# Kernel tuning notes

Measured on AMD Instinct MI355X. Metric: run time of the kernel, lower is better.

Reference implementation:

```python
import jax, jax.numpy as jnp
import numpy as np
from jax import lax

B, S, D, H_HEADS, K, G, E, HID = 2, 1024, 1024, 16, 31, 4, 2, 2048
HD = D // H_HEADS

def _layer_norm(x, g, b, eps=1e-5):
    mu = jnp.mean(x, axis=-1, keepdims=True)
    var = jnp.mean(jnp.square(x - mu), axis=-1, keepdims=True)
    return (x - mu) * lax.rsqrt(var + eps) * g + b

def setup_inputs() -> dict:
    key = jax.random.key(0)
    ks = jax.random.split(key, 16)
    s = 0.02
    return {
        "x": jax.random.normal(ks[0], (B, S, D), jnp.float32),
        "group_ids": jax.random.randint(ks[1], (B, S), 0, G, jnp.int32),
        "cn_g": jnp.ones((D,), jnp.float32), "cn_b": jnp.zeros((D,), jnp.float32),
        "conv_w": jax.random.normal(ks[2], (D, D, K), jnp.float32) * s,
        "conv_b": jnp.zeros((D,), jnp.float32),
        "an_g": jnp.ones((D,), jnp.float32), "an_b": jnp.zeros((D,), jnp.float32),
        "in_w": jax.random.normal(ks[3], (3 * D, D), jnp.float32) * s,
        "in_b": jnp.zeros((3 * D,), jnp.float32),
        "out_w": jax.random.normal(ks[4], (D, D), jnp.float32) * s,
        "out_b": jnp.zeros((D,), jnp.float32),
        "e_w1": jax.random.normal(ks[5], (G, E, D, HID), jnp.float32) * s,
        "e_b1": jnp.zeros((G, E, HID), jnp.float32),
        "e_w2": jax.random.normal(ks[6], (G, E, HID, D), jnp.float32) * s,
        "e_b2": jnp.zeros((G, E, D), jnp.float32),
    }

def reference(x, group_ids, cn_g, cn_b, conv_w, conv_b, an_g, an_b,
              in_w, in_b, out_w, out_b, e_w1, e_b1, e_w2, e_b2):
    # ---- conv block (dropout off: deterministic/eval) ----
    residual = x
    h = _layer_norm(x, cn_g, cn_b)
    hc = jnp.transpose(h, (0, 2, 1))  # [B, D, S]
    hc = lax.conv_general_dilated(hc, conv_w, window_strides=(1,),
                                  padding=[(K // 2, K // 2)],
                                  dimension_numbers=("NCH", "OIH", "NCH"))
    hc = hc + conv_b[None, :, None]
    hc = jnp.transpose(hc, (0, 2, 1))
    x = jax.nn.gelu(hc, approximate=False) + residual
    # ---- self-attention block ----
    residual = x
    h = _layer_norm(x, an_g, an_b)
    qkv = h @ in_w.T + in_b  # [B, S, 3D]
    q, k, v = jnp.split(qkv, 3, axis=-1)
    q = q.reshape(B, S, H_HEADS, HD)
    k = k.reshape(B, S, H_HEADS, HD)
    v = v.reshape(B, S, H_HEADS, HD)
    scores = jnp.einsum("bqhd,bkhd->bhqk", q, k) / jnp.sqrt(jnp.float32(HD))
    attn = jax.nn.softmax(scores, axis=-1)
    ctx = jnp.einsum("bhqk,bkhd->bqhd", attn, v).reshape(B, S, D)
    x = ctx @ out_w.T + out_b + residual
    # ---- group-routed MoE (dense compute over groups, select by group id) ----
    residual = x
    xf = x.reshape(B * S, D)
    gid = group_ids.reshape(B * S)
    h1 = jax.nn.gelu(jnp.einsum("nd,gedh->ngeh", xf, e_w1) + e_b1, approximate=False)
    out_all = jnp.einsum("ngeh,gehd->nged", h1, e_w2) + e_b2  # [N, G, E, D]
    out_all = jnp.mean(out_all, axis=2)  # mean over experts in group -> [N, G, D]
    sel = jnp.take_along_axis(out_all, gid[:, None, None].astype(jnp.int32), axis=1)[:, 0]
    x = sel.reshape(B, S, D) + residual
    return x
```

## Files before the change

kernel.cpp:

```cpp
#include <hip/hip_runtime.h>
#include <hip/hip_bf16.h>
#include <math.h>

#define BB 2
#define SS 1024
#define DD 1024
#define HH 16
#define HDIM 64
#define KK 31
#define GG 4
#define EE 2
#define HIDN 2048
#define NTOK (BB*SS)
#define D3 (3*DD)

typedef unsigned short u16;
typedef __attribute__((ext_vector_type(8))) short s16x8;
typedef __attribute__((ext_vector_type(8))) unsigned short u16x8;
typedef __attribute__((ext_vector_type(4))) unsigned short u16x4;
typedef __attribute__((ext_vector_type(4))) float f32x4;
typedef __attribute__((ext_vector_type(2))) unsigned int u32x2;

__device__ __forceinline__ float gelu_f(float x) {
  return 0.5f * x * (1.0f + erff(x * 0.7071067811865475f));
}
__device__ __forceinline__ u16 f2bf(float f) {
  unsigned u = __builtin_bit_cast(unsigned, f);
  u = (u + 0x7fffu + ((u >> 16) & 1u)) >> 16;
  return (u16)u;
}
__device__ __forceinline__ float bf2f(u16 u) {
  return __builtin_bit_cast(float, ((unsigned)u) << 16);
}
__device__ __forceinline__ f32x4 MFMA16(s16x8 a, s16x8 b, f32x4 c) {
  return __builtin_amdgcn_mfma_f32_16x16x32_bf16(a, b, c, 0, 0, 0);
}
#define GLOAD16(gp, lp) __builtin_amdgcn_global_load_lds( \
    (const __attribute__((address_space(1))) void*)(gp),  \
    (__attribute__((address_space(3))) void*)(lp), 16, 0, 0)

__global__ void ln_kernel(const float* __restrict__ x, const float* __restrict__ g,
                          const float* __restrict__ b, u16* __restrict__ out) {
  const int row = blockIdx.x;
  const int tid = threadIdx.x;
  __shared__ float red[4];
  const float4 v = reinterpret_cast<const float4*>(x + (size_t)row * DD)[tid];
  float s = v.x + v.y + v.z + v.w;
  s += __shfl_down(s, 32); s += __shfl_down(s, 16); s += __shfl_down(s, 8);
  s += __shfl_down(s, 4);  s += __shfl_down(s, 2);  s += __shfl_down(s, 1);
  if ((tid & 63) == 0) red[tid >> 6] = s;
  __syncthreads();
  const float mean = (red[0] + red[1] + red[2] + red[3]) * (1.0f / DD);
  __syncthreads();
  const float4 d = make_float4(v.x - mean, v.y - mean, v.z - mean, v.w - mean);
  float sq = d.x*d.x + d.y*d.y + d.z*d.z + d.w*d.w;
  sq += __shfl_down(sq, 32); sq += __shfl_down(sq, 16); sq += __shfl_down(sq, 8);
  sq += __shfl_down(sq, 4);  sq += __shfl_down(sq, 2);  sq += __shfl_down(sq, 1);
  if ((tid & 63) == 0) red[tid >> 6] = sq;
  __syncthreads();
  const float var = (red[0] + red[1] + red[2] + red[3]) * (1.0f / DD);
  const float rstd = rsqrtf(var + 1e-5f);
  const float4 gv = reinterpret_cast<const float4*>(g)[tid];
  const float4 bv = reinterpret_cast<const float4*>(b)[tid];
  u16x4 o;
  o[0] = f2bf(d.x * rstd * gv.x + bv.x);
  o[1] = f2bf(d.y * rstd * gv.y + bv.y);
  o[2] = f2bf(d.z * rstd * gv.z + bv.z);
  o[3] = f2bf(d.w * rstd * gv.w + bv.w);
  *reinterpret_cast<u16x4*>(out + (size_t)row * DD + tid * 4) = o;
}

__global__ void prep_convw(const float* __restrict__ cw, u16* __restrict__ Wb) {
  const int o = blockIdx.x;
#pragma unroll
  for (int rep = 0; rep < 4; ++rep) {
    const int i = rep * 256 + threadIdx.x;
    const float* src = cw + ((size_t)o * DD + i) * KK;
    float wv[KK];
#pragma unroll
    for (int k = 0; k < KK; ++k) wv[k] = src[k];
#pragma unroll
    for (int k = 0; k < KK; ++k)
      Wb[((size_t)k * DD + o) * DD + i] = f2bf(wv[k]);
  }
}

__global__ void cvt_kernel(const float* __restrict__ in, u16* __restrict__ outp, int n4) {
  const int i = blockIdx.x * 256 + threadIdx.x;
  if (i < n4) {
    const float4 v = reinterpret_cast<const float4*>(in)[i];
    u16x4 o; o[0] = f2bf(v.x); o[1] = f2bf(v.y); o[2] = f2bf(v.z); o[3] = f2bf(v.w);
    reinterpret_cast<u16x4*>(outp)[i] = o;
  }
}

__global__ void tr_kernel(const float* __restrict__ src, u16* __restrict__ dst, int R, int C) {
  __shared__ float tile[32][33];
  const int c0 = blockIdx.x * 32, r0 = blockIdx.y * 32;
  const size_t base = (size_t)blockIdx.z * R * C;
  const int tx = threadIdx.x & 31, ty = threadIdx.x >> 5;
#pragma unroll
  for (int i = 0; i < 4; ++i)
    tile[ty + i * 8][tx] = src[base + (size_t)(r0 + ty + i * 8) * C + c0 + tx];
  __syncthreads();
#pragma unroll
  for (int i = 0; i < 4; ++i)
    dst[base + (size_t)(c0 + ty + i * 8) * R + r0 + tx] = f2bf(tile[tx][ty + i * 8]);
}

__global__ void vtr_kernel(const u16* __restrict__ qkvb, u16* __restrict__ Vt) {
  __shared__ u16 tile[32][40];
  const int k0 = blockIdx.x * 32, d0 = blockIdx.y * 32, bh = blockIdx.z;
  const int b = bh >> 4, h = bh & 15;
  const int tx = threadIdx.x & 31, ty = threadIdx.x >> 5;
#pragma unroll
  for (int i = 0; i < 4; ++i)
    tile[ty + i * 8][tx] =
        qkvb[(size_t)(b * SS + k0 + ty + i * 8) * D3 + 2 * DD + h * HDIM + d0 + tx];
  __syncthreads();
#pragma unroll
  for (int i = 0; i < 4; ++i)
    Vt[((size_t)(b * HH + h) * HDIM + d0 + ty + i * 8) * SS + k0 + tx] = tile[tx][ty + i * 8];
}

__global__ __launch_bounds__(512) void conv_kernel(const u16* __restrict__ hb,
                                                   const u16* __restrict__ Wb,
                                                   u16* __restrict__ P) {
  const int L = blockIdx.x;
  const int o_t = L & 7;
  const int rest = L >> 3;
  const int s_t = rest >> 1;
  const int z = rest & 1;
  const int b = s_t >> 3, sloc = s_t & 7;
  const int s0l = sloc * 128;
  const int o0 = o_t * 128;
  const int ibase = z * 512;
  const int tid = threadIdx.x, lane = tid & 63, w = tid >> 6;
  const int wm = (w >> 2) & 1, wn = (w >> 1) & 1, ksid = w & 1;
  const int q15 = lane & 15, g = lane >> 4;
  __shared__ __align__(16) u16 Ad[2][160 * 64];
  __shared__ __align__(16) u16 Bp[8][3][2048];
  const int rlo = (sloc == 0) ? 15 : 0;
  const int rhi = (sloc == 7) ? 143 : 158;
  if (sloc == 0)
    for (int i = tid; i < 15 * 64; i += 512) { Ad[0][i] = 0; Ad[1][i] = 0; }
  if (sloc == 7)
    for (int i = tid; i < 17 * 64; i += 512) { Ad[0][143 * 64 + i] = 0; Ad[1][143 * 64 + i] = 0; }
  auto stageA = [&](int buf, int i0) {
    for (int q = w; q < 20; q += 8) {
      const int r = q * 8 + (lane >> 3);
      const int c = (lane & 7) ^ (r & 7);
      if (r >= rlo && r < rhi)
        GLOAD16(hb + (size_t)(b * SS + s0l - 15 + r) * DD + i0 + c * 8, &Ad[buf][q * 512]);
    }
  };
  auto stageBp = [&](int slot, int k, int i0w) {
#pragma unroll
    for (int q = 0; q < 4; ++q) {
      const int j = lane >> 2;
      const int r = q * 16 + j;
      const int c16 = (lane & 3) ^ ((j >> 1) & 3);
      GLOAD16(Wb + ((size_t)k * DD + o0 + wn * 64 + r) * DD + i0w + c16 * 8,
              &Bp[w][slot][q * 512]);
    }
  };
  f32x4 acc[4][4];
#pragma unroll
  for (int i = 0; i < 4; ++i)
#pragma unroll
    for (int j = 0; j < 4; ++j) acc[i][j] = f32x4{0.f, 0.f, 0.f, 0.f};
  const int ib0 = ibase + ksid * 32;
  stageA(0, ibase);
  stageBp(0, 0, ib0);
  stageBp(1, 1, ib0);
  asm volatile("s_waitcnt vmcnt(0)" ::: "memory");
  __syncthreads();
  const int T = 8 * KK;
  const int kx = ksid * 64;
  const int bro = q15 * 64 + ((g ^ ((q15 >> 1) & 3)) << 4);
  int t = 0;
  for (int i0i = 0; i0i < 8; ++i0i) {
    const u16* Ab = Ad[i0i & 1];
    for (int k = 0; k < KK; ++k, ++t) {
      {
        const int tn = t + 2;
        if (tn < T) stageBp(tn % 3, tn % KK, ibase + (tn / KK) * 64 + ksid * 32);
      }
      s16x8 af[4];
      const int rk0 = wm * 64 + q15 + k;
#pragma unroll
      for (int mf = 0; mf < 4; ++mf) {
        const int rr = rk0 + mf * 16;
        const char* p = (const char*)Ab + rr * 128;
        af[mf] = *(const s16x8*)(p + (((g ^ (rr & 7)) * 16) ^ kx));
      }
      if (t + 2 < T)      asm volatile("s_waitcnt vmcnt(8)" ::: "memory");
      else if (t + 1 < T) asm volatile("s_waitcnt vmcnt(4)" ::: "memory");
      else                asm volatile("s_waitcnt vmcnt(0)" ::: "memory");
      if (k == 5 && i0i < 7) stageA((i0i + 1) & 1, ibase + (i0i + 1) * 64);
      const char* Bb = (const char*)&Bp[w][t % 3][0];
      s16x8 bfr[4];
#pragma unroll
      for (int nf = 0; nf < 4; ++nf)
        bfr[nf] = *(const s16x8*)(Bb + nf * 1024 + bro);
      __builtin_amdgcn_s_setprio(1);
#pragma unroll
      for (int mf = 0; mf < 4; ++mf)
#pragma unroll
        for (int nf = 0; nf < 4; ++nf)
          acc[mf][nf] = MFMA16(af[mf], bfr[nf], acc[mf][nf]);
      __builtin_amdgcn_s_setprio(0);
    }
    if (i0i < 7) {
      asm volatile("s_waitcnt vmcnt(0)" ::: "memory");
      __syncthreads();
    }
  }
  __syncthreads();
  float* scr = (float*)(&Bp[0][0][0]) + (wm * 2 + wn) * 4096;
  if (ksid == 1) {
#pragma unroll
    for (int mf = 0; mf < 4; ++mf)
#pragma unroll
      for (int nf = 0; nf < 4; ++nf) {
        const int col = nf * 16 + q15;
        *(f32x4*)&scr[col * 64 + ((mf * 16 + g * 4) ^ ((col & 7) << 3))] = acc[mf][nf];
      }
  }
  __syncthreads();
  if (ksid == 0) {
    u16* Pz = P + (size_t)z * NTOK * DD;
#pragma unroll
    for (int mf = 0; mf < 4; ++mf) {
      f32x4 sum[4];
#pragma unroll
      for (int nf = 0; nf < 4; ++nf) {
        const int col = nf * 16 + q15;
        const f32x4 o = *(const f32x4*)&scr[col * 64 + ((mf * 16 + g * 4) ^ ((col & 7) << 3))];
        sum[nf] = acc[mf][nf] + o;
      }
#pragma unroll
      for (int r = 0; r < 4; ++r) {
        const int srow = s0l + wm * 64 + mf * 16 + g * 4 + r;
        u16* orow = Pz + (size_t)(b * SS + srow) * DD + o0 + wn * 64;
#pragma unroll
        for (int nf = 0; nf < 4; ++nf)
          orow[nf * 16 + q15] = f2bf(sum[nf][r]);
      }
    }
  }
}

__global__ void combine_kernel(const u16* __restrict__ P, const float* __restrict__ cb,
                               const float* __restrict__ x, float* __restrict__ x1) {
  const int idx = blockIdx.x * 256 + threadIdx.x;
  const size_t base = (size_t)idx * 4;
  const int col = (int)(base & (DD - 1));
  const u16x4 p0 = *(const u16x4*)(P + base);
  const u16x4 p1 = *(const u16x4*)(P + (size_t)NTOK * DD + base);
  const float4 xv = *(const float4*)(x + base);
  const float4 cbv = *(const float4*)(cb + col);
  float4 o;
  o.x = gelu_f(bf2f(p0[0]) + bf2f(p1[0]) + cbv.x) + xv.x;
  o.y = gelu_f(bf2f(p0[1]) + bf2f(p1[1]) + cbv.y) + xv.y;
  o.z = gelu_f(bf2f(p0[2]) + bf2f(p1[2]) + cbv.z) + xv.z;
  o.w = gelu_f(bf2f(p0[3]) + bf2f(p1[3]) + cbv.w) + xv.w;
  *(float4*)(x1 + base) = o;
}

__global__ __launch_bounds__(256) void qkv_kernel(const u16* __restrict__ A, const u16* __restrict__ B,
                           const float* __restrict__ bias, u16* __restrict__ C) {
  const int n0 = blockIdx.x * 64, m0 = blockIdx.y * 128;
  const int tid = threadIdx.x, lane = tid & 63, w = tid >> 6;
  const int wm = w >> 1, wn = w & 1;
  __shared__ u16 As[3][128 * 64];
  __shared__ u16 Bs[3][64 * 64];
  f32x4 acc[4][2];
#pragma unroll
  for (int i = 0; i < 4; ++i)
#pragma unroll
    for (int j = 0; j < 2; ++j) acc[i][j] = f32x4{0.f, 0.f, 0.f, 0.f};
  auto stage = [&](int t, int buf) {
    const int k0 = t * 64;
#pragma unroll
    for (int q = 0; q < 4; ++q) {
      const int idx = w * 4 + q, r = idx * 8 + (lane >> 3), c = (lane & 7) ^ (r & 7);
      GLOAD16(A + (size_t)(m0 + r) * DD + k0 + c * 8, &As[buf][idx * 512]);
    }
#pragma unroll
    for (int q = 0; q < 2; ++q) {
      const int idx = w * 2 + q, r = idx * 8 + (lane >> 3), c = (lane & 7) ^ (r & 7);
      GLOAD16(B + (size_t)(n0 + r) * DD + k0 + c * 8, &Bs[buf][idx * 512]);
    }
  };
  stage(0, 0);
  stage(1, 1);
  const int T = DD / 64;
  for (int t = 0; t < T; ++t) {
    if (t + 1 < T) asm volatile("s_waitcnt vmcnt(6)" ::: "memory");
    else           asm volatile("s_waitcnt vmcnt(0)" ::: "memory");
    __builtin_amdgcn_s_barrier();
    asm volatile("" ::: "memory");
    if (t + 2 < T) stage(t + 2, (t + 2) % 3);
    const u16* Ab = As[t % 3];
    const u16* Bb = Bs[t % 3];
    const int xb = (((lane >> 4) ^ (lane & 7)) * 16);
    s16x8 af[4][2], bfr[2][2];
#pragma unroll
    for (int mf = 0; mf < 4; ++mf) {
      const char* p = (const char*)Ab + (wm * 64 + mf * 16 + (lane & 15)) * 128;
      af[mf][0] = *(const s16x8*)(p + xb);
      af[mf][1] = *(const s16x8*)(p + (xb ^ 64));
    }
#pragma unroll
    for (int nf = 0; nf < 2; ++nf) {
      const char* p = (const char*)Bb + (wn * 32 + nf * 16 + (lane & 15)) * 128;
      bfr[nf][0] = *(const s16x8*)(p + xb);
      bfr[nf][1] = *(const s16x8*)(p + (xb ^ 64));
    }
    __builtin_amdgcn_s_setprio(1);
#pragma unroll
    for (int ks = 0; ks < 2; ++ks)
#pragma unroll
      for (int mf = 0; mf < 4; ++mf)
#pragma unroll
        for (int nf = 0; nf < 2; ++nf)
          acc[mf][nf] = MFMA16(af[mf][ks], bfr[nf][ks], acc[mf][nf]);
    __builtin_amdgcn_s_setprio(0);
  }
#pragma unroll
  for (int mf = 0; mf < 4; ++mf)
#pragma unroll
    for (int rr = 0; rr < 4; ++rr) {
      const int row = m0 + wm * 64 + mf * 16 + (lane >> 4) * 4 + rr;
#pragma unroll
      for (int nf = 0; nf < 2; ++nf) {
        const int col = n0 + wn * 32 + nf * 16 + (lane & 15);
        C[(size_t)row * D3 + col] = f2bf(acc[mf][nf][rr] + bias[col]);
      }
    }
}

__global__ __launch_bounds__(256) void out_kernel(const u16* __restrict__ A, const u16* __restrict__ B,
                           const float* __restrict__ bias, const float* __restrict__ resid,
                           float* __restrict__ C, u16* __restrict__ x2g,
                           const int* __restrict__ inv) {
  const int n0 = blockIdx.x * 64, m0 = blockIdx.y * 128;
  const int tid = threadIdx.x, lane = tid & 63, w = tid >> 6;
  const int wm = w >> 1, wn = w & 1;
  __shared__ u16 As[3][128 * 64];
  __shared__ u16 Bs[3][64 * 64];
  f32x4 acc[4][2];
#pragma unroll
  for (int i = 0; i < 4; ++i)
#pragma unroll
    for (int j = 0; j < 2; ++j) acc[i][j] = f32x4{0.f, 0.f, 0.f, 0.f};
  auto stage = [&](int t, int buf) {
    const int k0 = t * 64;
#pragma unroll
    for (int q = 0; q < 4; ++q) {
      const int idx = w * 4 + q, r = idx * 8 + (lane >> 3), c = (lane & 7) ^ (r & 7);
      GLOAD16(A + (size_t)(m0 + r) * DD + k0 + c * 8, &As[buf][idx * 512]);
    }
#pragma unroll
    for (int q = 0; q < 2; ++q) {
      const int idx = w * 2 + q, r = idx * 8 + (lane >> 3), c = (lane & 7) ^ (r & 7);
      GLOAD16(B + (size_t)(n0 + r) * DD + k0 + c * 8, &Bs[buf][idx * 512]);
    }
  };
  stage(0, 0);
  stage(1, 1);
  const int T = DD / 64;
  for (int t = 0; t < T; ++t) {
    if (t + 1 < T) asm volatile("s_waitcnt vmcnt(6)" ::: "memory");
    else           asm volatile("s_waitcnt vmcnt(0)" ::: "memory");
    __builtin_amdgcn_s_barrier();
    asm volatile("" ::: "memory");
    if (t + 2 < T) stage(t + 2, (t + 2) % 3);
    const u16* Ab = As[t % 3];
    const u16* Bb = Bs[t % 3];
    const int xb = (((lane >> 4) ^ (lane & 7)) * 16);
    s16x8 af[4][2], bfr[2][2];
#pragma unroll
    for (int mf = 0; mf < 4; ++mf) {
      const char* p = (const char*)Ab + (wm * 64 + mf * 16 + (lane & 15)) * 128;
      af[mf][0] = *(const s16x8*)(p + xb);
      af[mf][1] = *(const s16x8*)(p + (xb ^ 64));
    }
#pragma unroll
    for (int nf = 0; nf < 2; ++nf) {
      const char* p = (const char*)Bb + (wn * 32 + nf * 16 + (lane & 15)) * 128;
      bfr[nf][0] = *(const s16x8*)(p + xb);
      bfr[nf][1] = *(const s16x8*)(p + (xb ^ 64));
    }
    __builtin_amdgcn_s_setprio(1);
#pragma unroll
    for (int ks = 0; ks < 2; ++ks)
#pragma unroll
      for (int mf = 0; mf < 4; ++mf)
#pragma unroll
        for (int nf = 0; nf < 2; ++nf)
          acc[mf][nf] = MFMA16(af[mf][ks], bfr[nf][ks], acc[mf][nf]);
    __builtin_amdgcn_s_setprio(0);
  }
#pragma unroll
  for (int mf = 0; mf < 4; ++mf)
#pragma unroll
    for (int rr = 0; rr < 4; ++rr) {
      const int row = m0 + wm * 64 + mf * 16 + (lane >> 4) * 4 + rr;
      const int slot = inv[row];
#pragma unroll
      for (int nf = 0; nf < 2; ++nf) {
        const int col = n0 + wn * 32 + nf * 16 + (lane & 15);
        const float v = acc[mf][nf][rr] + bias[col] + resid[(size_t)row * DD + col];
        C[(size_t)row * DD + col] = v;
        x2g[(size_t)slot * DD + col] = f2bf(v);
      }
    }
}

__global__ __launch_bounds__(512) void attn_kernel(const u16* __restrict__ qkv,
                                                   const u16* __restrict__ Vt,
                                                   u16* __restrict__ ctx) {
  const int q0 = blockIdx.x * 128, h = blockIdx.y, b = blockIdx.z;
  const int tid = threadIdx.x, lane = tid & 63, w = tid >> 6;
  const int q15 = lane & 15, g = lane >> 4, l7 = lane & 7;
  __shared__ u16 Q_lds[128 * 64];
  __shared__ u16 K_lds[2][64 * 64];
  __shared__ u16 V_lds[2][64 * 64];
  __shared__ u16 P_lds[8][16 * 72];
  __shared__ float s_lds[8][16];

#pragma unroll
  for (int q2 = 0; q2 < 2; ++q2) {
    const int idx = w * 2 + q2;
    const int r = idx * 8 + (lane >> 3);
    const int c = l7 ^ (r & 7);
    GLOAD16(qkv + (size_t)(b * SS + q0 + r) * D3 + h * HDIM + c * 8, &Q_lds[idx * 512]);
  }
  auto stageK = [&](int buf, int kt) {
    const int r = w * 8 + (lane >> 3);
    const int c = l7 ^ (r & 7);
    GLOAD16(qkv + (size_t)(b * SS + kt * 64 + r) * D3 + DD + h * HDIM + c * 8,
            &K_lds[buf][w * 512]);
  };
  auto stageV = [&](int buf, int kt) {
    const int r = w * 8 + (lane >> 3);
    const int c = l7 ^ (r & 7);
    GLOAD16(Vt + ((size_t)(b * HH + h) * HDIM + r) * SS + kt * 64 + c * 8,
            &V_lds[buf][w * 512]);
  };
  stageK(0, 0);
  stageV(0, 0);
  asm volatile("s_waitcnt vmcnt(0)" ::: "memory");
  __syncthreads();
  s16x8 bq[2];
#pragma unroll
  for (int ks = 0; ks < 2; ++ks)
    bq[ks] = *(const s16x8*)((const char*)Q_lds + (w * 16 + q15) * 128 + ((4 * ks + g) ^ l7) * 16);
  f32x4 oacc[4];
#pragma unroll
  for (int nf = 0; nf < 4; ++nf) oacc[nf] = f32x4{0.f, 0.f, 0.f, 0.f};
  float mrun = -3.0e38f, lrun = 0.0f;
  int buf = 0;
  for (int kt = 0; kt < 16; ++kt) {
    if (kt < 15) { stageK(buf ^ 1, kt + 1); stageV(buf ^ 1, kt + 1); }
    f32x4 st[4];
#pragma unroll
    for (int mf = 0; mf < 4; ++mf) st[mf] = f32x4{0.f, 0.f, 0.f, 0.f};
#pragma unroll
    for (int ks = 0; ks < 2; ++ks) {
#pragma unroll
      for (int mf = 0; mf < 4; ++mf) {
        const s16x8 ka = *(const s16x8*)((const char*)K_lds[buf] + (mf * 16 + q15) * 128 +
                                         ((4 * ks + g) ^ l7) * 16);
        st[mf] = MFMA16(ka, bq[ks], st[mf]);
      }
    }
    float t0[4][4];
    float cmax = -3.0e38f;
#pragma unroll
    for (int mf = 0; mf < 4; ++mf)
#pragma unroll
      for (int r = 0; r < 4; ++r) {
        const float v = st[mf][r] * 0.125f;
        t0[mf][r] = v;
        cmax = fmaxf(cmax, v);
      }
    cmax = fmaxf(cmax, __shfl_xor(cmax, 16));
    cmax = fmaxf(cmax, __shfl_xor(cmax, 32));
    const float mnew = fmaxf(mrun, cmax);
    const float scf = __expf(mrun - mnew);
    float psum = 0.f;
#pragma unroll
    for (int mf = 0; mf < 4; ++mf)
#pragma unroll
      for (int r = 0; r < 4; ++r) {
        const float p = __expf(t0[mf][r] - mnew);
        t0[mf][r] = p;
        psum += p;
      }
    psum += __shfl_xor(psum, 16);
    psum += __shfl_xor(psum, 32);
    lrun = lrun * scf + psum;
    mrun = mnew;
    s_lds[w][q15] = scf;
    u16* pw = &P_lds[w][0];
#pragma unroll
    for (int mf = 0; mf < 4; ++mf) {
      u32x2 pk;
      pk[0] = (unsigned)f2bf(t0[mf][0]) | ((unsigned)f2bf(t0[mf][1]) << 16);
      pk[1] = (unsigned)f2bf(t0[mf][2]) | ((unsigned)f2bf(t0[mf][3]) << 16);
      *(u32x2*)(pw + q15 * 72 + mf * 16 + g * 4) = pk;
    }
    asm volatile("s_waitcnt lgkmcnt(0)" ::: "memory");
    const f32x4 scv = *(const f32x4*)&s_lds[w][g * 4];
#pragma unroll
    for (int nf = 0; nf < 4; ++nf)
#pragma unroll
      for (int r = 0; r < 4; ++r) oacc[nf][r] *= scv[r];
#pragma unroll
    for (int ks = 0; ks < 2; ++ks) {
      const s16x8 pa = *(const s16x8*)(pw + q15 * 72 + ks * 32 + g * 8);
#pragma unroll
      for (int nf = 0; nf < 4; ++nf) {
        const s16x8 bv = *(const s16x8*)((const char*)V_lds[buf] + (nf * 16 + q15) * 128 +
                                         ((4 * ks + g) ^ l7) * 16);
        oacc[nf] = MFMA16(pa, bv, oacc[nf]);
      }
    }
    asm volatile("s_waitcnt vmcnt(0)" ::: "memory");
    __syncthreads();
    buf ^= 1;
  }
  const float linv = 1.0f / lrun;
  s_lds[w][q15] = linv;
  asm volatile("s_waitcnt lgkmcnt(0)" ::: "memory");
  const f32x4 lv = *(const f32x4*)&s_lds[w][g * 4];
#pragma unroll
  for (int nf = 0; nf < 4; ++nf)
#pragma unroll
    for (int r = 0; r < 4; ++r) {
      const int qg = q0 + w * 16 + g * 4 + r;
      ctx[(size_t)(b * SS + qg) * DD + h * HDIM + nf * 16 + q15] = f2bf(oacc[nf][r] * lv[r]);
    }
}

__global__ void zero_counts_kernel(int* c) { if (threadIdx.x < GG) c[threadIdx.x] = 0; }

__global__ void gather_kernel(const int* __restrict__ gid, int* __restrict__ counts,
                              int* __restrict__ gather) {
  const int n = blockIdx.x * 256 + threadIdx.x;
  if (n < NTOK) {
    const int g = gid[n];
    const int slot = atomicAdd(&counts[g], 1);
    gather[g * NTOK + slot] = n;
  }
}

__global__ void scan_kernel(const int* __restrict__ cnts, int* __restrict__ off) {
  if (threadIdx.x == 0) {
    int s = 0;
#pragma unroll
    for (int g = 0; g < GG; ++g) { off[g] = s; s += cnts[g]; }
    off[GG] = s;
  }
}

__global__ void pack_kernel(const int* __restrict__ gat, const int* __restrict__ cnts,
                            const int* __restrict__ off, int* __restrict__ gidx,
                            int* __restrict__ inv) {
  const int g = blockIdx.y;
  const int slot = blockIdx.x * 256 + threadIdx.x;
  if (slot < cnts[g]) {
    const int tok = gat[g * NTOK + slot];
    const int sg = off[g] + slot;
    gidx[sg] = tok;
    inv[tok] = sg;
  }
}

__global__ __launch_bounds__(256) void moe1_kernel(const u16* __restrict__ x2g, const u16* __restrict__ w1t,
                            const float* __restrict__ e_b1, const int* __restrict__ off,
                            const int* __restrict__ cnts, u16* __restrict__ h1) {
  const int ge = blockIdx.z, g = ge >> 1, e = ge & 1;
  const int cnt = cnts[g];
  const int m0 = blockIdx.y * 128;
  if (m0 >= cnt) return;
  const int base = off[g];
  const int n0 = blockIdx.x * 64;
  const u16* A = x2g + (size_t)base * DD;
  const u16* B = w1t + (size_t)ge * HIDN * DD;
  const int tid = threadIdx.x, lane = tid & 63, w = tid >> 6;
  const int wm = w >> 1, wn = w & 1;
  __shared__ u16 As[3][128 * 64];
  __shared__ u16 Bs[3][64 * 64];
  f32x4 acc[4][2];
#pragma unroll
  for (int i = 0; i < 4; ++i)
#pragma unroll
    for (int j = 0; j < 2; ++j) acc[i][j] = f32x4{0.f, 0.f, 0.f, 0.f};
  auto stage = [&](int t, int buf) {
    const int k0 = t * 64;
#pragma unroll
    for (int q = 0; q < 4; ++q) {
      const int idx = w * 4 + q, r = idx * 8 + (lane >> 3), c = (lane & 7) ^ (r & 7);
      int rg = m0 + r; if (rg > cnt - 1) rg = cnt - 1;
      GLOAD16(A + (size_t)rg * DD + k0 + c * 8, &As[buf][idx * 512]);
    }
#pragma unroll
    for (int q = 0; q < 2; ++q) {
      const int idx = w * 2 + q, r = idx * 8 + (lane >> 3), c = (lane & 7) ^ (r & 7);
      GLOAD16(B + (size_t)(n0 + r) * DD + k0 + c * 8, &Bs[buf][idx * 512]);
    }
  };
  stage(0, 0);
  stage(1, 1);
  const int T = DD / 64;
  for (int t = 0; t < T; ++t) {
    if (t + 1 < T) asm volatile("s_waitcnt vmcnt(6)" ::: "memory");
    else           asm volatile("s_waitcnt vmcnt(0)" ::: "memory");
    __builtin_amdgcn_s_barrier();
    asm volatile("" ::: "memory");
    if (t + 2 < T) stage(t + 2, (t + 2) % 3);
    const u16* Ab = As[t % 3];
    const u16* Bb = Bs[t % 3];
    const int xb = (((lane >> 4) ^ (lane & 7)) * 16);
    s16x8 af[4][2], bfr[2][2];
#pragma unroll
    for (int mf = 0; mf < 4; ++mf) {
      const char* p = (const char*)Ab + (wm * 64 + mf * 16 + (lane & 15)) * 128;
      af[mf][0] = *(const s16x8*)(p + xb);
      af[mf][1] = *(const s16x8*)(p + (xb ^ 64));
    }
#pragma unroll
    for (int nf = 0; nf < 2; ++nf) {
      const char* p = (const char*)Bb + (wn * 32 + nf * 16 + (lane & 15)) * 128;
      bfr[nf][0] = *(const s16x8*)(p + xb);
      bfr[nf][1] = *(const s16x8*)(p + (xb ^ 64));
    }
    __builtin_amdgcn_s_setprio(1);
#pragma unroll
    for (int ks = 0; ks < 2; ++ks)
#pragma unroll
      for (int mf = 0; mf < 4; ++mf)
#pragma unroll
        for (int nf = 0; nf < 2; ++nf)
          acc[mf][nf] = MFMA16(af[mf][ks], bfr[nf][ks], acc[mf][nf]);
    __builtin_amdgcn_s_setprio(0);
  }
  const float* b1 = e_b1 + (size_t)ge * HIDN;
#pragma unroll
  for (int mf = 0; mf < 4; ++mf)
#pragma unroll
    for (int rr = 0; rr < 4; ++rr) {
      const int rowg = m0 + wm * 64 + mf * 16 + (lane >> 4) * 4 + rr;
      if (rowg < cnt) {
        u16* orow = h1 + ((size_t)e * NTOK + base + rowg) * HIDN;
#pragma unroll
        for (int nf = 0; nf < 2; ++nf) {
          const int col = n0 + wn * 32 + nf * 16 + (lane & 15);
          orow[col] = f2bf(gelu_f(acc[mf][nf][rr] + b1[col]));
        }
      }
    }
}

__global__ __launch_bounds__(256) void moe2_kernel(const u16* __restrict__ h1, const u16* __restrict__ w2t,
                            const float* __restrict__ e_b2, const int* __restrict__ off,
                            const int* __restrict__ cnts, const int* __restrict__ gidx,
                            const float* __restrict__ x2, float* __restrict__ outp) {
  const int g = blockIdx.z;
  const int cnt = cnts[g];
  const int m0 = blockIdx.y * 128;
  if (m0 >= cnt) return;
  const int base = off[g];
  const int n0 = blockIdx.x * 64;
  const int tid = threadIdx.x, lane = tid & 63, w = tid >> 6;
  const int wm = w >> 1, wn = w & 1;
  __shared__ u16 As[3][128 * 64];
  __shared__ u16 Bs[3][64 * 64];
  f32x4 acc[4][2];
#pragma unroll
  for (int i = 0; i < 4; ++i)
#pragma unroll
    for (int j = 0; j < 2; ++j) acc[i][j] = f32x4{0.f, 0.f, 0.f, 0.f};
  auto stage = [&](int t, int buf) {
    const int e = t >> 5;
    const int k0 = (t & 31) * 64;
#pragma unroll
    for (int q = 0; q < 4; ++q) {
      const int idx = w * 4 + q, r = idx * 8 + (lane >> 3), c = (lane & 7) ^ (r & 7);
      int rg = m0 + r; if (rg > cnt - 1) rg = cnt - 1;
      GLOAD16(h1 + ((size_t)e * NTOK + base + rg) * HIDN + k0 + c * 8, &As[buf][idx * 512]);
    }
#pragma unroll
    for (int q = 0; q < 2; ++q) {
      const int idx = w * 2 + q, r = idx * 8 + (lane >> 3), c = (lane & 7) ^ (r & 7);
      GLOAD16(w2t + ((size_t)(g * EE + e) * DD + n0 + r) * HIDN + k0 + c * 8, &Bs[buf][idx * 512]);
    }
  };
  stage(0, 0);
  stage(1, 1);
  const int T = 64;
  for (int t = 0; t < T; ++t) {
    if (t + 1 < T) asm volatile("s_waitcnt vmcnt(6)" ::: "memory");
    else           asm volatile("s_waitcnt vmcnt(0)" ::: "memory");
    __builtin_amdgcn_s_barrier();
    asm volatile("" ::: "memory");
    if (t + 2 < T) stage(t + 2, (t + 2) % 3);
    const u16* Ab = As[t % 3];
    const u16* Bb = Bs[t % 3];
    const int xb = (((lane >> 4) ^ (lane & 7)) * 16);
    s16x8 af[4][2], bfr[2][2];
#pragma unroll
    for (int mf = 0; mf < 4; ++mf) {
      const char* p = (const char*)Ab + (wm * 64 + mf * 16 + (lane & 15)) * 128;
      af[mf][0] = *(const s16x8*)(p + xb);
      af[mf][1] = *(const s16x8*)(p + (xb ^ 64));
    }
#pragma unroll
    for (int nf = 0; nf < 2; ++nf) {
      const char* p = (const char*)Bb + (wn * 32 + nf * 16 + (lane & 15)) * 128;
      bfr[nf][0] = *(const s16x8*)(p + xb);
      bfr[nf][1] = *(const s16x8*)(p + (xb ^ 64));
    }
    __builtin_amdgcn_s_setprio(1);
#pragma unroll
    for (int ks = 0; ks < 2; ++ks)
#pragma unroll
      for (int mf = 0; mf < 4; ++mf)
#pragma unroll
        for (int nf = 0; nf < 2; ++nf)
          acc[mf][nf] = MFMA16(af[mf][ks], bfr[nf][ks], acc[mf][nf]);
    __builtin_amdgcn_s_setprio(0);
  }
  const float* b20 = e_b2 + (size_t)(g * EE + 0) * DD;
  const float* b21 = e_b2 + (size_t)(g * EE + 1) * DD;
#pragma unroll
  for (int mf = 0; mf < 4; ++mf)
#pragma unroll
    for (int rr = 0; rr < 4; ++rr) {
      const int rowg = m0 + wm * 64 + mf * 16 + (lane >> 4) * 4 + rr;
      if (rowg < cnt) {
        const int tok = gidx[base + rowg];
#pragma unroll
        for (int nf = 0; nf < 2; ++nf) {
          const int col = n0 + wn * 32 + nf * 16 + (lane & 15);
          outp[(size_t)tok * DD + col] =
              0.5f * acc[mf][nf][rr] + 0.5f * (b20[col] + b21[col]) + x2[(size_t)tok * DD + col];
        }
      }
    }
}

extern "C" void kernel_launch(void* const* d_in, const int* in_sizes, int n_in,
                              void* d_out, int out_size, void* d_ws, size_t ws_size,
                              hipStream_t stream) {
  (void)in_sizes; (void)n_in; (void)out_size; (void)ws_size;
  const float* x      = (const float*)d_in[0];
  const int*   gid    = (const int*)d_in[1];
  const float* cn_g   = (const float*)d_in[2];
  const float* cn_b   = (const float*)d_in[3];
  const float* conv_w = (const float*)d_in[4];
  const float* conv_b = (const float*)d_in[5];
  const float* an_g   = (const float*)d_in[6];
  const float* an_b   = (const float*)d_in[7];
  const float* in_w   = (const float*)d_in[8];
  const float* in_b   = (const float*)d_in[9];
  const float* out_w  = (const float*)d_in[10];
  const float* out_b  = (const float*)d_in[11];
  const float* e_w1   = (const float*)d_in[12];
  const float* e_b1   = (const float*)d_in[13];
  const float* e_w2   = (const float*)d_in[14];
  const float* e_b2   = (const float*)d_in[15];
  float* outp = (float*)d_out;

  char* wsp = (char*)d_ws;
  u16*   hb    = (u16*)(wsp);
  u16*   Pc    = (u16*)(wsp + (4ull << 20));
  float* x1    = (float*)(wsp + (12ull << 20));
  u16*   Wb    = (u16*)(wsp + (12ull << 20));
  u16*   qkvb  = (u16*)(wsp + (24ull << 20));
  u16*   inwb  = (u16*)(wsp + (40ull << 20));
  u16*   outwb = (u16*)(wsp + (40ull << 20));
  u16*   Vt    = (u16*)(wsp + (46ull << 20));
  u16*   ctxb  = hb;
  float* x2    = (float*)(wsp + (52ull << 20));
  int*   inv   = (int*)(wsp + (60ull << 20));
  u16*   x2g   = (u16*)(wsp + (64ull << 20));
  u16*   wgt   = (u16*)(wsp + (4ull << 20));
  u16*   h1    = (u16*)(wsp + (36ull << 20));
  int*   gat   = (int*)(wsp + (74ull << 20));
  int*   cnts  = gat + GG * NTOK;
  int*   offp  = cnts + GG;
  int*   gidx  = offp + (GG + 1);

  ln_kernel<<<NTOK, 256, 0, stream>>>(x, cn_g, cn_b, hb);
  prep_convw<<<1024, 256, 0, stream>>>(conv_w, Wb);
  conv_kernel<<<256, 512, 0, stream>>>(hb, Wb, Pc);
  combine_kernel<<<NTOK * DD / 1024, 256, 0, stream>>>(Pc, conv_b, x, x1);
  zero_counts_kernel<<<1, 64, 0, stream>>>(cnts);
  gather_kernel<<<NTOK / 256, 256, 0, stream>>>(gid, cnts, gat);
  scan_kernel<<<1, 64, 0, stream>>>(cnts, offp);
  pack_kernel<<<dim3(NTOK / 256, GG), 256, 0, stream>>>(gat, cnts, offp, gidx, inv);
  ln_kernel<<<NTOK, 256, 0, stream>>>(x1, an_g, an_b, hb);
  cvt_kernel<<<3072, 256, 0, stream>>>(in_w, inwb, 3 * DD * DD / 4);
  qkv_kernel<<<dim3(D3 / 64, NTOK / 128), 256, 0, stream>>>(hb, inwb, in_b, qkvb);
  vtr_kernel<<<dim3(SS / 32, HDIM / 32, BB * HH), 256, 0, stream>>>(qkvb, Vt);
  attn_kernel<<<dim3(SS / 128, HH, BB), 512, 0, stream>>>(qkvb, Vt, ctxb);
  cvt_kernel<<<1024, 256, 0, stream>>>(out_w, outwb, DD * DD / 4);
  out_kernel<<<dim3(DD / 64, NTOK / 128), 256, 0, stream>>>(ctxb, outwb, out_b, x1, x2, x2g, inv);
  tr_kernel<<<dim3(HIDN / 32, DD / 32, GG * EE), 256, 0, stream>>>(e_w1, wgt, DD, HIDN);
  moe1_kernel<<<dim3(HIDN / 64, NTOK / 128, GG * EE), 256, 0, stream>>>(x2g, wgt, e_b1, offp, cnts, h1);
  tr_kernel<<<dim3(DD / 32, HIDN / 32, GG * EE), 256, 0, stream>>>(e_w2, wgt, HIDN, DD);
  moe2_kernel<<<dim3(DD / 64, NTOK / 128, GG), 256, 0, stream>>>(h1, wgt, e_b2, offp, cnts, gidx, x2, outp);
}
```

Baseline: 493.1 us.

## Widen QKV and MoE1 GEMM tiles to 128x128 with double buffering; vectorize conv weight prep

```diff
diff --git a/kernel.cpp b/kernel.cpp
--- a/kernel.cpp
+++ b/kernel.cpp
@@ -72,16 +72,20 @@
 
 __global__ void prep_convw(const float* __restrict__ cw, u16* __restrict__ Wb) {
   const int o = blockIdx.x;
-#pragma unroll
-  for (int rep = 0; rep < 4; ++rep) {
-    const int i = rep * 256 + threadIdx.x;
-    const float* src = cw + ((size_t)o * DD + i) * KK;
-    float wv[KK];
-#pragma unroll
-    for (int k = 0; k < KK; ++k) wv[k] = src[k];
-#pragma unroll
-    for (int k = 0; k < KK; ++k)
-      Wb[((size_t)k * DD + o) * DD + i] = f2bf(wv[k]);
+  const int i4 = threadIdx.x * 4;
+  float wv[4][KK];
+#pragma unroll
+  for (int j = 0; j < 4; ++j) {
+    const float* src = cw + ((size_t)o * DD + i4 + j) * KK;
+#pragma unroll
+    for (int k = 0; k < KK; ++k) wv[j][k] = src[k];
+  }
+#pragma unroll
+  for (int k = 0; k < KK; ++k) {
+    u16x4 o4;
+    o4[0] = f2bf(wv[0][k]); o4[1] = f2bf(wv[1][k]);
+    o4[2] = f2bf(wv[2][k]); o4[3] = f2bf(wv[3][k]);
+    *(u16x4*)&Wb[((size_t)k * DD + o) * DD + i4] = o4;
   }
 }
 
@@ -270,16 +274,16 @@
 
 __global__ __launch_bounds__(256) void qkv_kernel(const u16* __restrict__ A, const u16* __restrict__ B,
                            const float* __restrict__ bias, u16* __restrict__ C) {
-  const int n0 = blockIdx.x * 64, m0 = blockIdx.y * 128;
+  const int n0 = blockIdx.x * 128, m0 = blockIdx.y * 128;
   const int tid = threadIdx.x, lane = tid & 63, w = tid >> 6;
   const int wm = w >> 1, wn = w & 1;
-  __shared__ u16 As[3][128 * 64];
-  __shared__ u16 Bs[3][64 * 64];
-  f32x4 acc[4][2];
+  __shared__ u16 As[2][128 * 64];
+  __shared__ u16 Bs[2][128 * 64];
+  f32x4 acc[4][4];
 #pragma unroll
   for (int i = 0; i < 4; ++i)
 #pragma unroll
-    for (int j = 0; j < 2; ++j) acc[i][j] = f32x4{0.f, 0.f, 0.f, 0.f};
+    for (int j = 0; j < 4; ++j) acc[i][j] = f32x4{0.f, 0.f, 0.f, 0.f};
   auto stage = [&](int t, int buf) {
     const int k0 = t * 64;
 #pragma unroll
@@ -288,24 +292,26 @@
       GLOAD16(A + (size_t)(m0 + r) * DD + k0 + c * 8, &As[buf][idx * 512]);
     }
 #pragma unroll
-    for (int q = 0; q < 2; ++q) {
-      const int idx = w * 2 + q, r = idx * 8 + (lane >> 3), c = (lane & 7) ^ (r & 7);
+    for (int q = 0; q < 4; ++q) {
+      const int idx = w * 4 + q, r = idx * 8 + (lane >> 3), c = (lane & 7) ^ (r & 7);
       GLOAD16(B + (size_t)(n0 + r) * DD + k0 + c * 8, &Bs[buf][idx * 512]);
     }
   };
   stage(0, 0);
-  stage(1, 1);
+  asm volatile("s_waitcnt vmcnt(0)" ::: "memory");
+  __syncthreads();
   const int T = DD / 64;
   for (int t = 0; t < T; ++t) {
-    if (t + 1 < T) asm volatile("s_waitcnt vmcnt(6)" ::: "memory");
-    else           asm volatile("s_waitcnt vmcnt(0)" ::: "memory");
-    __builtin_amdgcn_s_barrier();
-    asm volatile("" ::: "memory");
-    if (t + 2 < T) stage(t + 2, (t + 2) % 3);
-    const u16* Ab = As[t % 3];
-    const u16* Bb = Bs[t % 3];
+    if (t > 0) {
+      asm volatile("s_waitcnt vmcnt(0)" ::: "memory");
+      __builtin_amdgcn_s_barrier();
+      asm volatile("" ::: "memory");
+    }
+    if (t + 1 < T) stage(t + 1, (t + 1) & 1);
+    const u16* Ab = As[t & 1];
+    const u16* Bb = Bs[t & 1];
     const int xb = (((lane >> 4) ^ (lane & 7)) * 16);
-    s16x8 af[4][2], bfr[2][2];
+    s16x8 af[4][2], bfr[4][2];
 #pragma unroll
     for (int mf = 0; mf < 4; ++mf) {
       const char* p = (const char*)Ab + (wm * 64 + mf * 16 + (lane & 15)) * 128;
@@ -313,8 +319,8 @@
       af[mf][1] = *(const s16x8*)(p + (xb ^ 64));
     }
 #pragma unroll
-    for (int nf = 0; nf < 2; ++nf) {
-      const char* p = (const char*)Bb + (wn * 32 + nf * 16 + (lane & 15)) * 128;
+    for (int nf = 0; nf < 4; ++nf) {
+      const char* p = (const char*)Bb + (wn * 64 + nf * 16 + (lane & 15)) * 128;
       bfr[nf][0] = *(const s16x8*)(p + xb);
       bfr[nf][1] = *(const s16x8*)(p + (xb ^ 64));
     }
@@ -324,7 +330,7 @@
 #pragma unroll
       for (int mf = 0; mf < 4; ++mf)
 #pragma unroll
-        for (int nf = 0; nf < 2; ++nf)
+        for (int nf = 0; nf < 4; ++nf)
           acc[mf][nf] = MFMA16(af[mf][ks], bfr[nf][ks], acc[mf][nf]);
     __builtin_amdgcn_s_setprio(0);
   }
@@ -334,8 +340,8 @@
     for (int rr = 0; rr < 4; ++rr) {
       const int row = m0 + wm * 64 + mf * 16 + (lane >> 4) * 4 + rr;
 #pragma unroll
-      for (int nf = 0; nf < 2; ++nf) {
-        const int col = n0 + wn * 32 + nf * 16 + (lane & 15);
+      for (int nf = 0; nf < 4; ++nf) {
+        const int col = n0 + wn * 64 + nf * 16 + (lane & 15);
         C[(size_t)row * D3 + col] = f2bf(acc[mf][nf][rr] + bias[col]);
       }
     }
@@ -588,18 +594,18 @@
   const int m0 = blockIdx.y * 128;
   if (m0 >= cnt) return;
   const int base = off[g];
-  const int n0 = blockIdx.x * 64;
+  const int n0 = blockIdx.x * 128;
   const u16* A = x2g + (size_t)base * DD;
   const u16* B = w1t + (size_t)ge * HIDN * DD;
   const int tid = threadIdx.x, lane = tid & 63, w = tid >> 6;
   const int wm = w >> 1, wn = w & 1;
-  __shared__ u16 As[3][128 * 64];
-  __shared__ u16 Bs[3][64 * 64];
-  f32x4 acc[4][2];
+  __shared__ u16 As[2][128 * 64];
+  __shared__ u16 Bs[2][128 * 64];
+  f32x4 acc[4][4];
 #pragma unroll
   for (int i = 0; i < 4; ++i)
 #pragma unroll
-    for (int j = 0; j < 2; ++j) acc[i][j] = f32x4{0.f, 0.f, 0.f, 0.f};
+    for (int j = 0; j < 4; ++j) acc[i][j] = f32x4{0.f, 0.f, 0.f, 0.f};
   auto stage = [&](int t, int buf) {
     const int k0 = t * 64;
 #pragma unroll
@@ -609,24 +615,26 @@
       GLOAD16(A + (size_t)rg * DD + k0 + c * 8, &As[buf][idx * 512]);
     }
 #pragma unroll
-    for (int q = 0; q < 2; ++q) {
-      const int idx = w * 2 + q, r = idx * 8 + (lane >> 3), c = (lane & 7) ^ (r & 7);
+    for (int q = 0; q < 4; ++q) {
+      const int idx = w * 4 + q, r = idx * 8 + (lane >> 3), c = (lane & 7) ^ (r & 7);
       GLOAD16(B + (size_t)(n0 + r) * DD + k0 + c * 8, &Bs[buf][idx * 512]);
     }
   };
   stage(0, 0);
-  stage(1, 1);
+  asm volatile("s_waitcnt vmcnt(0)" ::: "memory");
+  __syncthreads();
   const int T = DD / 64;
   for (int t = 0; t < T; ++t) {
-    if (t + 1 < T) asm volatile("s_waitcnt vmcnt(6)" ::: "memory");
-    else           asm volatile("s_waitcnt vmcnt(0)" ::: "memory");
-    __builtin_amdgcn_s_barrier();
-    asm volatile("" ::: "memory");
-    if (t + 2 < T) stage(t + 2, (t + 2) % 3);
-    const u16* Ab = As[t % 3];
-    const u16* Bb = Bs[t % 3];
+    if (t > 0) {
+      asm volatile("s_waitcnt vmcnt(0)" ::: "memory");
+      __builtin_amdgcn_s_barrier();
+      asm volatile("" ::: "memory");
+    }
+    if (t + 1 < T) stage(t + 1, (t + 1) & 1);
+    const u16* Ab = As[t & 1];
+    const u16* Bb = Bs[t & 1];
     const int xb = (((lane >> 4) ^ (lane & 7)) * 16);
-    s16x8 af[4][2], bfr[2][2];
+    s16x8 af[4][2], bfr[4][2];
 #pragma unroll
     for (int mf = 0; mf < 4; ++mf) {
       const char* p = (const char*)Ab + (wm * 64 + mf * 16 + (lane & 15)) * 128;
@@ -634,8 +642,8 @@
       af[mf][1] = *(const s16x8*)(p + (xb ^ 64));
     }
 #pragma unroll
-    for (int nf = 0; nf < 2; ++nf) {
-      const char* p = (const char*)Bb + (wn * 32 + nf * 16 + (lane & 15)) * 128;
+    for (int nf = 0; nf < 4; ++nf) {
+      const char* p = (const char*)Bb + (wn * 64 + nf * 16 + (lane & 15)) * 128;
       bfr[nf][0] = *(const s16x8*)(p + xb);
       bfr[nf][1] = *(const s16x8*)(p + (xb ^ 64));
     }
@@ -645,7 +653,7 @@
 #pragma unroll
       for (int mf = 0; mf < 4; ++mf)
 #pragma unroll
-        for (int nf = 0; nf < 2; ++nf)
+        for (int nf = 0; nf < 4; ++nf)
           acc[mf][nf] = MFMA16(af[mf][ks], bfr[nf][ks], acc[mf][nf]);
     __builtin_amdgcn_s_setprio(0);
   }
@@ -658,8 +666,8 @@
       if (rowg < cnt) {
         u16* orow = h1 + ((size_t)e * NTOK + base + rowg) * HIDN;
 #pragma unroll
-        for (int nf = 0; nf < 2; ++nf) {
-          const int col = n0 + wn * 32 + nf * 16 + (lane & 15);
+        for (int nf = 0; nf < 4; ++nf) {
+          const int col = n0 + wn * 64 + nf * 16 + (lane & 15);
           orow[col] = f2bf(gelu_f(acc[mf][nf][rr] + b1[col]));
         }
       }
@@ -806,13 +814,13 @@
   pack_kernel<<<dim3(NTOK / 256, GG), 256, 0, stream>>>(gat, cnts, offp, gidx, inv);
   ln_kernel<<<NTOK, 256, 0, stream>>>(x1, an_g, an_b, hb);
   cvt_kernel<<<3072, 256, 0, stream>>>(in_w, inwb, 3 * DD * DD / 4);
-  qkv_kernel<<<dim3(D3 / 64, NTOK / 128), 256, 0, stream>>>(hb, inwb, in_b, qkvb);
+  qkv_kernel<<<dim3(D3 / 128, NTOK / 128), 256, 0, stream>>>(hb, inwb, in_b, qkvb);
   vtr_kernel<<<dim3(SS / 32, HDIM / 32, BB * HH), 256, 0, stream>>>(qkvb, Vt);
   attn_kernel<<<dim3(SS / 128, HH, BB), 512, 0, stream>>>(qkvb, Vt, ctxb);
   cvt_kernel<<<1024, 256, 0, stream>>>(out_w, outwb, DD * DD / 4);
   out_kernel<<<dim3(DD / 64, NTOK / 128), 256, 0, stream>>>(ctxb, outwb, out_b, x1, x2, x2g, inv);
   tr_kernel<<<dim3(HIDN / 32, DD / 32, GG * EE), 256, 0, stream>>>(e_w1, wgt, DD, HIDN);
-  moe1_kernel<<<dim3(HIDN / 64, NTOK / 128, GG * EE), 256, 0, stream>>>(x2g, wgt, e_b1, offp, cnts, h1);
+  moe1_kernel<<<dim3(HIDN / 128, NTOK / 128, GG * EE), 256, 0, stream>>>(x2g, wgt, e_b1, offp, cnts, h1);
   tr_kernel<<<dim3(DD / 32, HIDN / 32, GG * EE), 256, 0, stream>>>(e_w2, wgt, HIDN, DD);
   moe2_kernel<<<dim3(DD / 64, NTOK / 128, GG), 256, 0, stream>>>(h1, wgt, e_b2, offp, cnts, gidx, x2, outp);
 }
```

New measurement: 489.4 us. Within noise of the previous version (-0.7%).
